# Performance work log

Hardware: AMD Instinct MI355X
Metric: run time of the kernel (lower is better)

The kernel has to match this reference:

```python
import jax, jax.numpy as jnp
import numpy as np

B, T, E = 4, 2048, 2048
H, KV = 16, 4
G = H // KV           # GQA group size
D = E // H            # head_dim = 128


def setup_inputs() -> dict:
    key = jax.random.key(0)
    kx, kq, kk, kv, ko = jax.random.split(key, 5)
    s = 1.0 / np.sqrt(E).astype(np.float32)
    x  = jax.random.normal(kx, (B, T, E), jnp.float32)
    Wq = jax.random.normal(kq, (E, H * D), jnp.float32) * s
    Wk = jax.random.normal(kk, (E, KV * D), jnp.float32) * s
    Wv = jax.random.normal(kv, (E, KV * D), jnp.float32) * s
    Wo = jax.random.normal(ko, (H * D, E), jnp.float32) * s
    return {"x": x, "Wq": Wq, "Wk": Wk, "Wv": Wv, "Wo": Wo}


def reference(x, Wq, Wk, Wv, Wo):
    # causal=True (default in the torch module)
    b, t, _ = x.shape
    scale = 1.0 / np.sqrt(D).astype(np.float32)
    # q heads ordered so that reshape (H,)->(KV,G) matches torch repeat_interleave
    q = (x @ Wq).reshape(b, t, KV, G, D)   # (B,T,KV,G,D)
    k = (x @ Wk).reshape(b, t, KV, D)      # (B,T,KV,D)
    v = (x @ Wv).reshape(b, t, KV, D)
    # scores per (kv-head h, group member g): (B,KV,G,T,T)
    scores = jnp.einsum('bqhgd,bkhd->bhgqk', q, k) * scale
    causal_mask = jnp.tril(jnp.ones((t, t), dtype=bool))  # True = keep
    scores = jnp.where(causal_mask, scores, -jnp.inf)
    w = jax.nn.softmax(scores, axis=-1)
    y = jnp.einsum('bhgqk,bkhd->bqhgd', w, v)  # (B,T,KV,G,D)
    y = y.reshape(b, t, H * D)
    return y @ Wo
```

## Files before the change

kernel.cpp:

```cpp
#include <hip/hip_runtime.h>

typedef unsigned short u16;
typedef __attribute__((ext_vector_type(8))) __bf16 bf16x8;
typedef __attribute__((ext_vector_type(4))) float f32x4;

#define BB 4
#define TT 2048
#define EE 2048
#define HH 16
#define KVH 4
#define DD 128

static __device__ __forceinline__ u16 f2bf(float f) {
  unsigned int u = __float_as_uint(f);
  u += 0x7fffu + ((u >> 16) & 1u);
  return (u16)(u >> 16);
}

static __device__ __forceinline__ void gl_lds16(const u16* g, u16* l) {
  __builtin_amdgcn_global_load_lds((__attribute__((address_space(1))) void*)g,
                                   (__attribute__((address_space(3))) void*)l,
                                   16, 0, 0);
}

__global__ __launch_bounds__(256) void cvt_f32_bf16(const float* __restrict__ in,
                                                    u16* __restrict__ out, int n4) {
  int i = blockIdx.x * 256 + threadIdx.x;
  if (i >= n4) return;
  float4 v = ((const float4*)in)[i];
  union { uint2 u2; u16 s[4]; } o;
  o.s[0] = f2bf(v.x); o.s[1] = f2bf(v.y); o.s[2] = f2bf(v.z); o.s[3] = f2bf(v.w);
  ((uint2*)out)[i] = o.u2;
}

__global__ __launch_bounds__(256) void transpose_w(const float* __restrict__ W,
                                                   u16* __restrict__ Wt, int R, int C) {
  __shared__ float tile[32][33];
  int tx = threadIdx.x & 31, ty = threadIdx.x >> 5;
  int r0 = blockIdx.y * 32, c0 = blockIdx.x * 32;
  #pragma unroll
  for (int i = ty; i < 32; i += 8)
    tile[i][tx] = W[(size_t)(r0 + i) * C + (c0 + tx)];
  __syncthreads();
  #pragma unroll
  for (int i = ty; i < 32; i += 8)
    Wt[(size_t)(c0 + i) * R + (r0 + tx)] = f2bf(tile[tx][i]);
}

__global__ __launch_bounds__(256) void transpose_v(const u16* __restrict__ KVb,
                                                   u16* __restrict__ VTg) {
  __shared__ u16 tile[32][36];
  const int tid = threadIdx.x;
  const int t0 = blockIdx.x * 32, d0 = blockIdx.y * 32;
  const int z = blockIdx.z;
  const int vb = z * 128;
  const size_t srcbase = (size_t)(z >> 2) * TT * 1024 + 512 + (z & 3) * 128;
  {
    int i = tid >> 3, c4 = (tid & 7) * 4;
    union { uint2 u; u16 s[4]; } r;
    r.u = *(const uint2*)(KVb + srcbase + (size_t)(t0 + i) * 1024 + d0 + c4);
    tile[i][c4] = r.s[0]; tile[i][c4 + 1] = r.s[1];
    tile[i][c4 + 2] = r.s[2]; tile[i][c4 + 3] = r.s[3];
  }
  __syncthreads();
  {
    int j = tid >> 3, cc = (tid & 7) * 4;
    union { uint2 u; u16 s[4]; } w;
    w.s[0] = tile[cc][j]; w.s[1] = tile[cc + 1][j];
    w.s[2] = tile[cc + 2][j]; w.s[3] = tile[cc + 3][j];
    *(uint2*)(VTg + (size_t)(vb + d0 + j) * TT + t0 + cc) = w.u;
  }
}

template <int BF16OUT>
__global__ __launch_bounds__(256) void gemm_bt(const u16* __restrict__ A,
                                               const u16* __restrict__ Bt,
                                               void* __restrict__ Cv,
                                               int M, int N, int K) {
  __shared__ u16 As[128 * 32];
  __shared__ u16 Bs[128 * 32];
  const int tid = threadIdx.x;
  const int lane = tid & 63, wave = tid >> 6;
  const int quad = lane >> 4, n16 = lane & 15;
  const int wm = (wave >> 1) * 64, wn = (wave & 1) * 64;
  const size_t rowbase = (size_t)blockIdx.y * 128;
  const size_t colbase = (size_t)blockIdx.x * 128;

  f32x4 acc[4][4];
  #pragma unroll
  for (int i = 0; i < 4; ++i)
    #pragma unroll
    for (int j = 0; j < 4; ++j)
      acc[i][j] = (f32x4){0.f, 0.f, 0.f, 0.f};

  const int srow = tid >> 2;
  const int scol = (tid & 3) * 8;
  const u16* Ag = A + (rowbase + srow) * (size_t)K + scol;
  const u16* Bg = Bt + (colbase + srow) * (size_t)K + scol;
  u16* Asd0 = &As[srow * 32 + scol];
  u16* Asd1 = &As[(srow + 64) * 32 + scol];
  u16* Bsd0 = &Bs[srow * 32 + scol];
  u16* Bsd1 = &Bs[(srow + 64) * 32 + scol];

  for (int kb = 0; kb < K; kb += 32) {
    __syncthreads();
    gl_lds16(Ag + kb, Asd0);
    gl_lds16(Ag + (size_t)64 * K + kb, Asd1);
    gl_lds16(Bg + kb, Bsd0);
    gl_lds16(Bg + (size_t)64 * K + kb, Bsd1);
    __syncthreads();

    bf16x8 af[4], bfr[4];
    #pragma unroll
    for (int mt = 0; mt < 4; ++mt)
      af[mt] = *(const bf16x8*)&As[(wm + mt * 16 + n16) * 32 + quad * 8];
    #pragma unroll
    for (int nt = 0; nt < 4; ++nt)
      bfr[nt] = *(const bf16x8*)&Bs[(wn + nt * 16 + n16) * 32 + quad * 8];
    #pragma unroll
    for (int mt = 0; mt < 4; ++mt)
      #pragma unroll
      for (int nt = 0; nt < 4; ++nt)
        acc[mt][nt] = __builtin_amdgcn_mfma_f32_16x16x32_bf16(af[mt], bfr[nt], acc[mt][nt], 0, 0, 0);
  }

  #pragma unroll
  for (int mt = 0; mt < 4; ++mt) {
    #pragma unroll
    for (int r = 0; r < 4; ++r) {
      size_t row = rowbase + wm + mt * 16 + quad * 4 + r;
      #pragma unroll
      for (int nt = 0; nt < 4; ++nt) {
        size_t col = colbase + wn + nt * 16 + n16;
        float v = acc[mt][nt][r];
        if (BF16OUT) ((u16*)Cv)[row * N + col] = f2bf(v);
        else         ((float*)Cv)[row * N + col] = v;
      }
    }
  }
}

__global__ __launch_bounds__(256) void attn_kernel(const u16* __restrict__ Qm,
                                                   const u16* __restrict__ KVm,
                                                   const u16* __restrict__ VTg,
                                                   u16* __restrict__ Ym) {
  __shared__ u16 Ks[32 * 128];
  __shared__ u16 Vt[128 * 32];
  __shared__ u16 Pb[4 * 32 * 40];

  const int tid = threadIdx.x;
  const int lane = tid & 63, wave = tid >> 6;
  const int quad = lane >> 4, n16 = lane & 15;
  const int b = blockIdx.y >> 4, h = blockIdx.y & 15;
  const int kvh = h >> 2;
  const int kvbase = b * TT;
  const u16* VTg_ = VTg + (size_t)((b * 4 + kvh) * 128) * TT;

  const int krow = tid >> 4;
  const int kslot = tid & 15;
  const int kg = (kslot ^ krow) * 8;
  u16* Ksd0 = &Ks[krow * 128 + kslot * 8];
  u16* Ksd1 = &Ks[(krow + 16) * 128 + kslot * 8];
  const int vrow = tid >> 2, vc = (tid & 3) * 8;
  u16* Vtd0 = &Vt[vrow * 32 + vc];
  u16* Vtd1 = &Vt[(vrow + 64) * 32 + vc];

  constexpr float SCL = 0.08838834764831843f * 1.4426950408889634f;

  for (int pass = 0; pass < 2; ++pass) {
    const int qt = pass ? 15 - (int)blockIdx.x : (int)blockIdx.x;
    const int q0 = qt * 128;
    const size_t qrowbase = (size_t)(b * TT + q0);
    const int wq0 = wave * 32;

    bf16x8 aq[2][4];
    #pragma unroll
    for (int mt = 0; mt < 2; ++mt) {
      const u16* qp = Qm + (qrowbase + wq0 + mt * 16 + n16) * (HH * DD) + h * DD + quad * 8;
      #pragma unroll
      for (int dt = 0; dt < 4; ++dt)
        aq[mt][dt] = *(const bf16x8*)(qp + dt * 32);
    }

    float lrow[2][4];
    f32x4 oacc[2][8];
    #pragma unroll
    for (int mt = 0; mt < 2; ++mt) {
      #pragma unroll
      for (int r = 0; r < 4; ++r) lrow[mt][r] = 0.f;
      #pragma unroll
      for (int i = 0; i < 8; ++i) oacc[mt][i] = (f32x4){0.f, 0.f, 0.f, 0.f};
    }

    const int kend = q0 + 128;
    for (int kb = 0; kb < kend; kb += 32) {
      __syncthreads();
      gl_lds16(KVm + (size_t)(kvbase + kb + krow) * 1024 + kvh * DD + kg, Ksd0);
      gl_lds16(KVm + (size_t)(kvbase + kb + krow + 16) * 1024 + kvh * DD + kg, Ksd1);
      gl_lds16(VTg_ + (size_t)vrow * TT + kb + vc, Vtd0);
      gl_lds16(VTg_ + (size_t)(vrow + 64) * TT + kb + vc, Vtd1);
      __syncthreads();

      f32x4 sf[2][2];
      #pragma unroll
      for (int half = 0; half < 2; ++half) {
        bf16x8 bk[4];
        #pragma unroll
        for (int dt = 0; dt < 4; ++dt) {
          int slot = (dt * 4 + quad) ^ n16;
          bk[dt] = *(const bf16x8*)&Ks[(half * 16 + n16) * 128 + slot * 8];
        }
        #pragma unroll
        for (int mt = 0; mt < 2; ++mt) {
          f32x4 s = (f32x4){0.f, 0.f, 0.f, 0.f};
          #pragma unroll
          for (int dt = 0; dt < 4; ++dt)
            s = __builtin_amdgcn_mfma_f32_16x16x32_bf16(aq[mt][dt], bk[dt], s, 0, 0, 0);
          sf[mt][half] = s;
        }
      }

      u16* pw = &Pb[wave * (32 * 40)];
      #pragma unroll
      for (int mt = 0; mt < 2; ++mt)
        #pragma unroll
        for (int half = 0; half < 2; ++half) {
          int key = kb + half * 16 + n16;
          #pragma unroll
          for (int r = 0; r < 4; ++r) {
            int qpos = q0 + wq0 + mt * 16 + quad * 4 + r;
            float pv = (key <= qpos) ? exp2f(sf[mt][half][r] * SCL) : 0.f;
            lrow[mt][r] += pv;
            pw[(mt * 16 + quad * 4 + r) * 40 + half * 16 + n16] = f2bf(pv);
          }
        }
      __builtin_amdgcn_s_waitcnt(0);
      bf16x8 ap[2];
      ap[0] = *(const bf16x8*)&pw[n16 * 40 + quad * 8];
      ap[1] = *(const bf16x8*)&pw[(16 + n16) * 40 + quad * 8];

      #pragma unroll
      for (int dt = 0; dt < 8; ++dt) {
        bf16x8 bv = *(const bf16x8*)&Vt[(dt * 16 + n16) * 32 + quad * 8];
        oacc[0][dt] = __builtin_amdgcn_mfma_f32_16x16x32_bf16(ap[0], bv, oacc[0][dt], 0, 0, 0);
        oacc[1][dt] = __builtin_amdgcn_mfma_f32_16x16x32_bf16(ap[1], bv, oacc[1][dt], 0, 0, 0);
      }
    }

    float rinv[2][4];
    #pragma unroll
    for (int mt = 0; mt < 2; ++mt)
      #pragma unroll
      for (int r = 0; r < 4; ++r) {
        float v = lrow[mt][r];
        v += __shfl_xor(v, 1, 64);
        v += __shfl_xor(v, 2, 64);
        v += __shfl_xor(v, 4, 64);
        v += __shfl_xor(v, 8, 64);
        rinv[mt][r] = 1.0f / v;
      }
    #pragma unroll
    for (int mt = 0; mt < 2; ++mt)
      #pragma unroll
      for (int dt = 0; dt < 8; ++dt)
        #pragma unroll
        for (int r = 0; r < 4; ++r) {
          size_t row = qrowbase + wq0 + mt * 16 + quad * 4 + r;
          Ym[row * (HH * DD) + h * DD + dt * 16 + n16] = f2bf(oacc[mt][dt][r] * rinv[mt][r]);
        }
  }
}

extern "C" void kernel_launch(void* const* d_in, const int* in_sizes, int n_in,
                              void* d_out, int out_size, void* d_ws, size_t ws_size,
                              hipStream_t stream) {
  const float* x  = (const float*)d_in[0];
  const float* Wq = (const float*)d_in[1];
  const float* Wk = (const float*)d_in[2];
  const float* Wv = (const float*)d_in[3];
  const float* Wo = (const float*)d_in[4];
  float* out = (float*)d_out;

  u16* ws   = (u16*)d_ws;
  u16* xb   = ws;
  u16* Wbuf = xb + (size_t)8192 * 2048;
  u16* Yb   = xb;

  u16* ob   = (u16*)d_out;
  u16* Qb   = ob;
  u16* KVb  = ob + (size_t)8192 * 2048;
  u16* VTg  = ob + (size_t)8192 * 2048 + (size_t)8192 * 1024;

  cvt_f32_bf16<<<16384, 256, 0, stream>>>(x, xb, (4 * 2048 * 2048) / 4);

  transpose_w<<<dim3(64, 64), 256, 0, stream>>>(Wq, Wbuf, 2048, 2048);
  gemm_bt<1><<<dim3(16, 64), 256, 0, stream>>>(xb, Wbuf, (void*)Qb, 8192, 2048, 2048);

  transpose_w<<<dim3(16, 64), 256, 0, stream>>>(Wk, Wbuf, 2048, 512);
  transpose_w<<<dim3(16, 64), 256, 0, stream>>>(Wv, Wbuf + (size_t)512 * 2048, 2048, 512);
  gemm_bt<1><<<dim3(8, 64), 256, 0, stream>>>(xb, Wbuf, (void*)KVb, 8192, 1024, 2048);

  transpose_v<<<dim3(64, 4, 16), 256, 0, stream>>>(KVb, VTg);

  attn_kernel<<<dim3(8, 64), 256, 0, stream>>>(Qb, KVb, VTg, Yb);

  transpose_w<<<dim3(64, 64), 256, 0, stream>>>(Wo, Wbuf, 2048, 2048);
  gemm_bt<0><<<dim3(16, 64), 256, 0, stream>>>(Yb, Wbuf, (void*)out, 8192, 2048, 2048);
}
```

Before: 574.4 us.

## Split attention into one q-tile per block and fold softmax scale into Q projection

```diff
diff --git a/kernel.cpp b/kernel.cpp
--- a/kernel.cpp
+++ b/kernel.cpp
@@ -15,6 +15,9 @@
   unsigned int u = __float_as_uint(f);
   u += 0x7fffu + ((u >> 16) & 1u);
   return (u16)(u >> 16);
+}
+static __device__ __forceinline__ u16 f2bf_tr(float f) {
+  return (u16)(__float_as_uint(f) >> 16);
 }
 
 static __device__ __forceinline__ void gl_lds16(const u16* g, u16* l) {
@@ -76,7 +79,7 @@
 __global__ __launch_bounds__(256) void gemm_bt(const u16* __restrict__ A,
                                                const u16* __restrict__ Bt,
                                                void* __restrict__ Cv,
-                                               int M, int N, int K) {
+                                               int M, int N, int K, float cmul) {
   __shared__ u16 As[128 * 32];
   __shared__ u16 Bs[128 * 32];
   const int tid = threadIdx.x;
@@ -132,7 +135,7 @@
       #pragma unroll
       for (int nt = 0; nt < 4; ++nt) {
         size_t col = colbase + wn + nt * 16 + n16;
-        float v = acc[mt][nt][r];
+        float v = acc[mt][nt][r] * cmul;
         if (BF16OUT) ((u16*)Cv)[row * N + col] = f2bf(v);
         else         ((float*)Cv)[row * N + col] = v;
       }
@@ -165,62 +168,71 @@
   u16* Vtd0 = &Vt[vrow * 32 + vc];
   u16* Vtd1 = &Vt[(vrow + 64) * 32 + vc];
 
-  constexpr float SCL = 0.08838834764831843f * 1.4426950408889634f;
-
-  for (int pass = 0; pass < 2; ++pass) {
-    const int qt = pass ? 15 - (int)blockIdx.x : (int)blockIdx.x;
-    const int q0 = qt * 128;
-    const size_t qrowbase = (size_t)(b * TT + q0);
-    const int wq0 = wave * 32;
-
-    bf16x8 aq[2][4];
-    #pragma unroll
-    for (int mt = 0; mt < 2; ++mt) {
-      const u16* qp = Qm + (qrowbase + wq0 + mt * 16 + n16) * (HH * DD) + h * DD + quad * 8;
-      #pragma unroll
-      for (int dt = 0; dt < 4; ++dt)
-        aq[mt][dt] = *(const bf16x8*)(qp + dt * 32);
-    }
-
-    float lrow[2][4];
-    f32x4 oacc[2][8];
-    #pragma unroll
-    for (int mt = 0; mt < 2; ++mt) {
-      #pragma unroll
-      for (int r = 0; r < 4; ++r) lrow[mt][r] = 0.f;
-      #pragma unroll
-      for (int i = 0; i < 8; ++i) oacc[mt][i] = (f32x4){0.f, 0.f, 0.f, 0.f};
-    }
-
-    const int kend = q0 + 128;
-    for (int kb = 0; kb < kend; kb += 32) {
-      __syncthreads();
-      gl_lds16(KVm + (size_t)(kvbase + kb + krow) * 1024 + kvh * DD + kg, Ksd0);
-      gl_lds16(KVm + (size_t)(kvbase + kb + krow + 16) * 1024 + kvh * DD + kg, Ksd1);
-      gl_lds16(VTg_ + (size_t)vrow * TT + kb + vc, Vtd0);
-      gl_lds16(VTg_ + (size_t)(vrow + 64) * TT + kb + vc, Vtd1);
-      __syncthreads();
-
-      f32x4 sf[2][2];
-      #pragma unroll
-      for (int half = 0; half < 2; ++half) {
-        bf16x8 bk[4];
+  const int qt = 15 - (int)blockIdx.x;
+  const int q0 = qt * 128;
+  const size_t qrowbase = (size_t)(b * TT + q0);
+  const int wq0 = wave * 32;
+
+  bf16x8 aq[2][4];
+  #pragma unroll
+  for (int mt = 0; mt < 2; ++mt) {
+    const u16* qp = Qm + (qrowbase + wq0 + mt * 16 + n16) * (HH * DD) + h * DD + quad * 8;
+    #pragma unroll
+    for (int dt = 0; dt < 4; ++dt)
+      aq[mt][dt] = *(const bf16x8*)(qp + dt * 32);
+  }
+
+  float lrow[2][4];
+  f32x4 oacc[2][8];
+  #pragma unroll
+  for (int mt = 0; mt < 2; ++mt) {
+    #pragma unroll
+    for (int r = 0; r < 4; ++r) lrow[mt][r] = 0.f;
+    #pragma unroll
+    for (int i = 0; i < 8; ++i) oacc[mt][i] = (f32x4){0.f, 0.f, 0.f, 0.f};
+  }
+
+  const int kend = q0 + 128;
+  for (int kb = 0; kb < kend; kb += 32) {
+    __syncthreads();
+    gl_lds16(KVm + (size_t)(kvbase + kb + krow) * 1024 + kvh * DD + kg, Ksd0);
+    gl_lds16(KVm + (size_t)(kvbase + kb + krow + 16) * 1024 + kvh * DD + kg, Ksd1);
+    gl_lds16(VTg_ + (size_t)vrow * TT + kb + vc, Vtd0);
+    gl_lds16(VTg_ + (size_t)(vrow + 64) * TT + kb + vc, Vtd1);
+    __syncthreads();
+
+    f32x4 sf[2][2];
+    #pragma unroll
+    for (int half = 0; half < 2; ++half) {
+      bf16x8 bk[4];
+      #pragma unroll
+      for (int dt = 0; dt < 4; ++dt) {
+        int slot = (dt * 4 + quad) ^ n16;
+        bk[dt] = *(const bf16x8*)&Ks[(half * 16 + n16) * 128 + slot * 8];
+      }
+      #pragma unroll
+      for (int mt = 0; mt < 2; ++mt) {
+        f32x4 s = (f32x4){0.f, 0.f, 0.f, 0.f};
         #pragma unroll
-        for (int dt = 0; dt < 4; ++dt) {
-          int slot = (dt * 4 + quad) ^ n16;
-          bk[dt] = *(const bf16x8*)&Ks[(half * 16 + n16) * 128 + slot * 8];
-        }
+        for (int dt = 0; dt < 4; ++dt)
+          s = __builtin_amdgcn_mfma_f32_16x16x32_bf16(aq[mt][dt], bk[dt], s, 0, 0, 0);
+        sf[mt][half] = s;
+      }
+    }
+
+    u16* pw = &Pb[wave * (32 * 40)];
+    if (kb + 31 <= q0 + wq0) {
+      #pragma unroll
+      for (int mt = 0; mt < 2; ++mt)
         #pragma unroll
-        for (int mt = 0; mt < 2; ++mt) {
-          f32x4 s = (f32x4){0.f, 0.f, 0.f, 0.f};
+        for (int half = 0; half < 2; ++half)
           #pragma unroll
-          for (int dt = 0; dt < 4; ++dt)
-            s = __builtin_amdgcn_mfma_f32_16x16x32_bf16(aq[mt][dt], bk[dt], s, 0, 0, 0);
-          sf[mt][half] = s;
-        }
-      }
-
-      u16* pw = &Pb[wave * (32 * 40)];
+          for (int r = 0; r < 4; ++r) {
+            float pv = exp2f(sf[mt][half][r]);
+            lrow[mt][r] += pv;
+            pw[(mt * 16 + quad * 4 + r) * 40 + half * 16 + n16] = f2bf_tr(pv);
+          }
+    } else {
       #pragma unroll
       for (int mt = 0; mt < 2; ++mt)
         #pragma unroll
@@ -229,46 +241,46 @@
           #pragma unroll
           for (int r = 0; r < 4; ++r) {
             int qpos = q0 + wq0 + mt * 16 + quad * 4 + r;
-            float pv = (key <= qpos) ? exp2f(sf[mt][half][r] * SCL) : 0.f;
+            float pv = (key <= qpos) ? exp2f(sf[mt][half][r]) : 0.f;
             lrow[mt][r] += pv;
-            pw[(mt * 16 + quad * 4 + r) * 40 + half * 16 + n16] = f2bf(pv);
+            pw[(mt * 16 + quad * 4 + r) * 40 + half * 16 + n16] = f2bf_tr(pv);
           }
         }
-      __builtin_amdgcn_s_waitcnt(0);
-      bf16x8 ap[2];
-      ap[0] = *(const bf16x8*)&pw[n16 * 40 + quad * 8];
-      ap[1] = *(const bf16x8*)&pw[(16 + n16) * 40 + quad * 8];
-
-      #pragma unroll
-      for (int dt = 0; dt < 8; ++dt) {
-        bf16x8 bv = *(const bf16x8*)&Vt[(dt * 16 + n16) * 32 + quad * 8];
-        oacc[0][dt] = __builtin_amdgcn_mfma_f32_16x16x32_bf16(ap[0], bv, oacc[0][dt], 0, 0, 0);
-        oacc[1][dt] = __builtin_amdgcn_mfma_f32_16x16x32_bf16(ap[1], bv, oacc[1][dt], 0, 0, 0);
+    }
+    __builtin_amdgcn_s_waitcnt(0xC07F);
+    bf16x8 ap[2];
+    ap[0] = *(const bf16x8*)&pw[n16 * 40 + quad * 8];
+    ap[1] = *(const bf16x8*)&pw[(16 + n16) * 40 + quad * 8];
+
+    #pragma unroll
+    for (int dt = 0; dt < 8; ++dt) {
+      bf16x8 bv = *(const bf16x8*)&Vt[(dt * 16 + n16) * 32 + quad * 8];
+      oacc[0][dt] = __builtin_amdgcn_mfma_f32_16x16x32_bf16(ap[0], bv, oacc[0][dt], 0, 0, 0);
+      oacc[1][dt] = __builtin_amdgcn_mfma_f32_16x16x32_bf16(ap[1], bv, oacc[1][dt], 0, 0, 0);
+    }
+  }
+
+  float rinv[2][4];
+  #pragma unroll
+  for (int mt = 0; mt < 2; ++mt)
+    #pragma unroll
+    for (int r = 0; r < 4; ++r) {
+      float v = lrow[mt][r];
+      v += __shfl_xor(v, 1, 64);
+      v += __shfl_xor(v, 2, 64);
+      v += __shfl_xor(v, 4, 64);
+      v += __shfl_xor(v, 8, 64);
+      rinv[mt][r] = 1.0f / v;
+    }
+  #pragma unroll
+  for (int mt = 0; mt < 2; ++mt)
+    #pragma unroll
+    for (int dt = 0; dt < 8; ++dt)
+      #pragma unroll
+      for (int r = 0; r < 4; ++r) {
+        size_t row = qrowbase + wq0 + mt * 16 + quad * 4 + r;
+        Ym[row * (HH * DD) + h * DD + dt * 16 + n16] = f2bf(oacc[mt][dt][r] * rinv[mt][r]);
       }
-    }
-
-    float rinv[2][4];
-    #pragma unroll
-    for (int mt = 0; mt < 2; ++mt)
-      #pragma unroll
-      for (int r = 0; r < 4; ++r) {
-        float v = lrow[mt][r];
-        v += __shfl_xor(v, 1, 64);
-        v += __shfl_xor(v, 2, 64);
-        v += __shfl_xor(v, 4, 64);
-        v += __shfl_xor(v, 8, 64);
-        rinv[mt][r] = 1.0f / v;
-      }
-    #pragma unroll
-    for (int mt = 0; mt < 2; ++mt)
-      #pragma unroll
-      for (int dt = 0; dt < 8; ++dt)
-        #pragma unroll
-        for (int r = 0; r < 4; ++r) {
-          size_t row = qrowbase + wq0 + mt * 16 + quad * 4 + r;
-          Ym[row * (HH * DD) + h * DD + dt * 16 + n16] = f2bf(oacc[mt][dt][r] * rinv[mt][r]);
-        }
-  }
 }
 
 extern "C" void kernel_launch(void* const* d_in, const int* in_sizes, int n_in,
@@ -291,19 +303,21 @@
   u16* KVb  = ob + (size_t)8192 * 2048;
   u16* VTg  = ob + (size_t)8192 * 2048 + (size_t)8192 * 1024;
 
+  const float SCL = 0.08838834764831843f * 1.4426950408889634f;
+
   cvt_f32_bf16<<<16384, 256, 0, stream>>>(x, xb, (4 * 2048 * 2048) / 4);
 
   transpose_w<<<dim3(64, 64), 256, 0, stream>>>(Wq, Wbuf, 2048, 2048);
-  gemm_bt<1><<<dim3(16, 64), 256, 0, stream>>>(xb, Wbuf, (void*)Qb, 8192, 2048, 2048);
+  gemm_bt<1><<<dim3(16, 64), 256, 0, stream>>>(xb, Wbuf, (void*)Qb, 8192, 2048, 2048, SCL);
 
   transpose_w<<<dim3(16, 64), 256, 0, stream>>>(Wk, Wbuf, 2048, 512);
   transpose_w<<<dim3(16, 64), 256, 0, stream>>>(Wv, Wbuf + (size_t)512 * 2048, 2048, 512);
-  gemm_bt<1><<<dim3(8, 64), 256, 0, stream>>>(xb, Wbuf, (void*)KVb, 8192, 1024, 2048);
+  gemm_bt<1><<<dim3(8, 64), 256, 0, stream>>>(xb, Wbuf, (void*)KVb, 8192, 1024, 2048, 1.0f);
 
   transpose_v<<<dim3(64, 4, 16), 256, 0, stream>>>(KVb, VTg);
 
-  attn_kernel<<<dim3(8, 64), 256, 0, stream>>>(Qb, KVb, VTg, Yb);
+  attn_kernel<<<dim3(16, 64), 256, 0, stream>>>(Qb, KVb, VTg, Yb);
 
   transpose_w<<<dim3(64, 64), 256, 0, stream>>>(Wo, Wbuf, 2048, 2048);
-  gemm_bt<0><<<dim3(16, 64), 256, 0, stream>>>(Yb, Wbuf, (void*)out, 8192, 2048, 2048);
-}
+  gemm_bt<0><<<dim3(16, 64), 256, 0, stream>>>(Yb, Wbuf, (void*)out, 8192, 2048, 2048, 1.0f);
+}
```

New measurement: 615.6 us. 7.2% more time.
